# Kernel tuning notes

Measured on AMD Instinct MI355X. Metric: run time of the kernel, lower is better.

Reference implementation:

```python
import jax, jax.numpy as jnp
import numpy as np

N = 100000   # num_labels
E = 3200000  # num edges
F_IN, H1, H2 = 384, 128, 64


def setup_inputs() -> dict:
    key = jax.random.key(0)
    k0, k1, k2, k3 = jax.random.split(key, 4)
    x = jax.random.normal(k0, (N, F_IN), dtype=jnp.float32) * 0.05
    W1 = jax.random.normal(k1, (F_IN, H1), dtype=jnp.float32) * (1.0 / np.sqrt(F_IN))
    b1 = jnp.zeros((H1,), dtype=jnp.float32)
    W2 = jax.random.normal(k2, (H1, H2), dtype=jnp.float32) * (1.0 / np.sqrt(H1))
    b2 = jnp.zeros((H2,), dtype=jnp.float32)
    edge_index = jax.random.randint(k3, (2, E), 0, N, dtype=jnp.int32)
    return {"x": x, "W1": W1, "b1": b1, "W2": W2, "b2": b2, "edge_index": edge_index}


def _gcn_norm(edge_index, num_nodes):
    # PyG gcn_norm: add self loops, deg from dst with unit weights, sym norm.
    loops = jnp.arange(num_nodes, dtype=edge_index.dtype)
    src = jnp.concatenate([edge_index[0], loops])
    dst = jnp.concatenate([edge_index[1], loops])
    deg = jax.ops.segment_sum(jnp.ones_like(dst, dtype=jnp.float32), dst,
                              num_segments=num_nodes)
    dis = jnp.where(deg > 0, jax.lax.rsqrt(deg), 0.0)
    norm = dis[src] * dis[dst]  # [E + N]
    return src, dst, norm


def _gcn_conv(x, W, b, src, dst, norm, num_nodes):
    h = x @ W                                   # [N, out]
    msg = h[src] * norm[:, None]                # gather + scale
    out = jax.ops.segment_sum(msg, dst, num_segments=num_nodes)
    return out + b


def reference(x, W1, b1, W2, b2, edge_index):
    src, dst, norm = _gcn_norm(edge_index, N)
    h = jax.nn.relu(_gcn_conv(x, W1, b1, src, dst, norm, N))
    out = _gcn_conv(h, W2, b2, src, dst, norm, N)
    return out
```

## Files before the change

### kernel.cpp

```cpp
#include <hip/hip_runtime.h>
#include <hip/hip_fp16.h>
#include <math.h>

#define N_NODES 100000
#define N_EDGES 3200000
#define F_IN    384
#define H1      128
#define H2      64

#define NBKT    782
#define HIST_W  800
#define NB_BIN  256
#define EPB     (N_EDGES / NB_BIN)


__global__ __launch_bounds__(256) void k_hist(const int* __restrict__ dst,
                                              int* __restrict__ hist) {
    __shared__ int h[HIST_W];
    int b = blockIdx.x, t = threadIdx.x;
    for (int i = t; i < HIST_W; i += 256) h[i] = 0;
    __syncthreads();
    int e0 = b * EPB, e1 = e0 + EPB;
    for (int e = e0 + t; e < e1; e += 256)
        atomicAdd(&h[dst[e] >> 7], 1);
    __syncthreads();
    for (int i = t; i < HIST_W; i += 256) hist[b * HIST_W + i] = h[i];
}


__global__ __launch_bounds__(1024) void k_scan_off(int* __restrict__ hist,
                                                   int* __restrict__ bucketBase) {
    __shared__ int s[1024];
    int t = threadIdx.x;
    int run = 0;
    if (t < HIST_W) {
        #pragma unroll 8
        for (int b = 0; b < NB_BIN; b++) {
            int v = hist[b * HIST_W + t];
            hist[b * HIST_W + t] = run;
            run += v;
        }
    }
    int tot = (t < NBKT) ? run : 0;
    s[t] = tot; __syncthreads();
    for (int off = 1; off < 1024; off <<= 1) {
        int x = (t >= off) ? s[t - off] : 0;
        __syncthreads();
        s[t] += x;
        __syncthreads();
    }
    if (t <= NBKT) bucketBase[t] = s[t] - tot;
}


__global__ __launch_bounds__(256) void k_bin(const int* __restrict__ src,
                                             const int* __restrict__ dst,
                                             const int* __restrict__ hist,
                                             const int* __restrict__ bucketBase,
                                             int* __restrict__ binned) {
    __shared__ int lcur[HIST_W];
    int b = blockIdx.x, t = threadIdx.x;
    for (int i = t; i < HIST_W; i += 256)
        lcur[i] = ((i < NBKT) ? bucketBase[i] : 0) + hist[b * HIST_W + i];
    __syncthreads();
    int e0 = b * EPB, e1 = e0 + EPB;
    for (int e = e0 + t; e < e1; e += 256) {
        int d = dst[e];
        int p = atomicAdd(&lcur[d >> 7], 1);
        binned[p] = ((d & 127) << 17) | src[e];
    }
}


__global__ __launch_bounds__(256) void k_build(const int* __restrict__ binned,
                                               const int* __restrict__ bucketBase,
                                               int* __restrict__ csr,
                                               int* __restrict__ offsets,
                                               int* __restrict__ ecnt,
                                               float* __restrict__ dis) {
    __shared__ int ldeg[128], spre[128], lcur[128];
    int bkt = blockIdx.x, t = threadIdx.x;
    int e0 = bucketBase[bkt], e1 = bucketBase[bkt + 1];
    if (t < 128) ldeg[t] = 0;
    __syncthreads();
    for (int e = e0 + t; e < e1; e += 256)
        atomicAdd(&ldeg[binned[e] >> 17], 1);
    __syncthreads();
    int v = (t < 128) ? ldeg[t] : 0;
    if (t < 128) spre[t] = v;
    __syncthreads();
    for (int off = 1; off < 128; off <<= 1) {
        int x = (t < 128 && t >= off) ? spre[t - off] : 0;
        __syncthreads();
        if (t < 128) spre[t] += x;
        __syncthreads();
    }
    if (t < 128) {
        int node = bkt * 128 + t;
        if (node < N_NODES) {
            int base = e0 + spre[t] - v;
            offsets[node] = base;
            ecnt[node]    = v;
            dis[node]     = rsqrtf((float)(v + 1));
            lcur[t]       = base;
        }
    }
    __syncthreads();
    for (int e = e0 + t; e < e1; e += 256) {
        int p = binned[e];
        int pos = atomicAdd(&lcur[p >> 17], 1);
        csr[pos] = p & 0x1FFFF;
    }
}


__global__ __launch_bounds__(256) void k_gemm1(const float* __restrict__ x,
                                               const float* __restrict__ W1,
                                               const float* __restrict__ dis,
                                               __half* __restrict__ hs1) {
    __shared__ float xl[16][72];
    __shared__ float wl[16][128];
    int t = threadIdx.x;
    int m0 = blockIdx.x * 64;
    int tr = t >> 5, tc = t & 31;
    float acc[8][4] = {};
    for (int k0 = 0; k0 < F_IN; k0 += 16) {
        {
            int r = t >> 2, kq = (t & 3) * 4;
            int rr = m0 + r; if (rr >= N_NODES) rr = N_NODES - 1;
            float4 a = *(const float4*)&x[(size_t)rr * F_IN + k0 + kq];
            xl[kq][r] = a.x; xl[kq + 1][r] = a.y; xl[kq + 2][r] = a.z; xl[kq + 3][r] = a.w;
        }
        #pragma unroll
        for (int jj = 0; jj < 2; jj++) {
            int idx = t + jj * 256;
            int k = idx >> 5, c4 = idx & 31;
            *(float4*)&wl[k][c4 * 4] = *(const float4*)&W1[(size_t)(k0 + k) * H1 + c4 * 4];
        }
        __syncthreads();
        #pragma unroll
        for (int kk = 0; kk < 16; kk++) {
            float4 a0 = *(const float4*)&xl[kk][tr * 8];
            float4 a1 = *(const float4*)&xl[kk][tr * 8 + 4];
            float4 b  = *(const float4*)&wl[kk][tc * 4];
            float av[8] = {a0.x, a0.y, a0.z, a0.w, a1.x, a1.y, a1.z, a1.w};
            float bv[4] = {b.x, b.y, b.z, b.w};
            #pragma unroll
            for (int i = 0; i < 8; i++)
                #pragma unroll
                for (int u = 0; u < 4; u++)
                    acc[i][u] += av[i] * bv[u];
        }
        __syncthreads();
    }
    #pragma unroll
    for (int i = 0; i < 8; i++) {
        int row = m0 + tr * 8 + i;
        if (row < N_NODES) {
            float dr = dis[row];
            __half2* o2 = (__half2*)&hs1[(size_t)row * H1 + tc * 4];
            o2[0] = __floats2half2_rn(acc[i][0] * dr, acc[i][1] * dr);
            o2[1] = __floats2half2_rn(acc[i][2] * dr, acc[i][3] * dr);
        }
    }
}


__global__ __launch_bounds__(256) void k_agg1(const __half* __restrict__ hs1,
                                              const float* __restrict__ dis,
                                              const int* __restrict__ csr,
                                              const int* __restrict__ offsets,
                                              const int* __restrict__ ecnt,
                                              const float* __restrict__ b1,
                                              float* __restrict__ hr) {
    int w = (blockIdx.x * 256 + threadIdx.x) >> 6;
    if (w >= N_NODES) return;
    int lane = threadIdx.x & 63;
    int j = lane * 2;
    const __half2* __restrict__ h = (const __half2*)hs1;
    float di = dis[w];
    int start = offsets[w];
    int cnt = ecnt[w];
    float2 selfv = __half22float2(h[(size_t)w * 64 + lane]);
    float sx = selfv.x;
    float sy = selfv.y;
    for (int k = 0; k < cnt; k += 8) {
        int s[8]; __half2 v[8];
        #pragma unroll
        for (int u = 0; u < 8; u++) {
            int kk = k + u;
            s[u] = csr[start + (kk < cnt ? kk : cnt - 1)];
        }
        #pragma unroll
        for (int u = 0; u < 8; u++)
            v[u] = h[(size_t)s[u] * 64 + lane];
        #pragma unroll
        for (int u = 0; u < 8; u++) {
            float2 f = __half22float2(v[u]);
            bool ok = (k + u < cnt);
            sx += ok ? f.x : 0.f;
            sy += ok ? f.y : 0.f;
        }
    }
    float2 bb = *(const float2*)&b1[j];
    float2 o = make_float2(fmaxf(bb.x + di * sx, 0.f),
                           fmaxf(bb.y + di * sy, 0.f));
    *(float2*)&hr[(size_t)w * H1 + j] = o;
}


__global__ __launch_bounds__(256) void k_gemm2(const float* __restrict__ hr,
                                               const float* __restrict__ W2,
                                               const float* __restrict__ dis,
                                               __half* __restrict__ hs2) {
    __shared__ float hl[32][128];
    __shared__ float wl[128][64];
    int t = threadIdx.x;
    int m0 = blockIdx.x * 32;
    #pragma unroll
    for (int j = 0; j < 8; j++) {
        int i4 = t + j * 256;
        int r = i4 >> 4, c4 = i4 & 15;
        *(float4*)&wl[r][c4 * 4] = *(const float4*)&W2[(size_t)r * H2 + c4 * 4];
    }
    #pragma unroll
    for (int j = 0; j < 4; j++) {
        int i4 = t + j * 256;
        int r = i4 >> 5, c4 = i4 & 31;
        *(float4*)&hl[r][c4 * 4] = *(const float4*)&hr[(size_t)(m0 + r) * H1 + c4 * 4];
    }
    __syncthreads();
    int c = t & 63, rg = t >> 6;
    float acc[8] = {};
    for (int k = 0; k < H1; k++) {
        float wv = wl[k][c];
        #pragma unroll
        for (int i = 0; i < 8; i++) acc[i] += hl[rg * 8 + i][k] * wv;
    }
    #pragma unroll
    for (int i = 0; i < 8; i++) {
        int row = m0 + rg * 8 + i;
        hs2[(size_t)row * H2 + c] = __float2half_rn(dis[row] * acc[i]);
    }
}


__global__ __launch_bounds__(256) void k_agg2(const __half* __restrict__ hs2,
                                              const float* __restrict__ dis,
                                              const int* __restrict__ csr,
                                              const int* __restrict__ offsets,
                                              const int* __restrict__ ecnt,
                                              const float* __restrict__ b2,
                                              float* __restrict__ out) {
    int w = (blockIdx.x * 256 + threadIdx.x) >> 6;
    if (w >= N_NODES) return;
    int lane = threadIdx.x & 63;
    float di = dis[w];
    int start = offsets[w];
    int cnt = ecnt[w];
    float acc = __half2float(hs2[(size_t)w * H2 + lane]);
    for (int k = 0; k < cnt; k += 8) {
        int s[8]; __half v[8];
        #pragma unroll
        for (int u = 0; u < 8; u++) {
            int kk = k + u;
            s[u] = csr[start + (kk < cnt ? kk : cnt - 1)];
        }
        #pragma unroll
        for (int u = 0; u < 8; u++)
            v[u] = hs2[(size_t)s[u] * H2 + lane];
        #pragma unroll
        for (int u = 0; u < 8; u++) {
            float f = __half2float(v[u]);
            acc += (k + u < cnt) ? f : 0.f;
        }
    }
    out[(size_t)w * H2 + lane] = b2[lane] + di * acc;
}


extern "C" void kernel_launch(void* const* d_in, const int* in_sizes, int n_in,
                              void* d_out, int out_size, void* d_ws, size_t ws_size,
                              hipStream_t stream) {
    const float* x  = (const float*)d_in[0];
    const float* W1 = (const float*)d_in[1];
    const float* b1 = (const float*)d_in[2];
    const float* W2 = (const float*)d_in[3];
    const float* b2 = (const float*)d_in[4];
    const int*   ei = (const int*)d_in[5];
    const int* src = ei;
    const int* dst = ei + N_EDGES;
    float* out = (float*)d_out;

    char* ws = (char*)d_ws;
    float* dis        = (float*)ws; ws += (size_t)N_NODES * 4;
    int*   offsets    = (int*)ws;   ws += (size_t)N_NODES * 4;
    int*   ecnt       = (int*)ws;   ws += (size_t)N_NODES * 4;
    int*   bucketBase = (int*)ws;   ws += 1024 * 4;
    int*   hist       = (int*)ws;   ws += (size_t)NB_BIN * HIST_W * 4;
    int*   csr        = (int*)ws;   ws += (size_t)N_EDGES * 4;
    __half* hs1       = (__half*)ws; ws += (size_t)N_NODES * H1 * 2;
    float* hr         = (float*)ws; ws += (size_t)N_NODES * H1 * 4;
    int*   binned     = (int*)hr;
    __half* hs2       = hs1;

    k_hist    <<<NB_BIN, 256, 0, stream>>>(dst, hist);
    k_scan_off<<<1, 1024, 0, stream>>>(hist, bucketBase);
    k_bin     <<<NB_BIN, 256, 0, stream>>>(src, dst, hist, bucketBase, binned);
    k_build   <<<NBKT, 256, 0, stream>>>(binned, bucketBase, csr, offsets, ecnt, dis);

    k_gemm1<<<(N_NODES + 63) / 64, 256, 0, stream>>>(x, W1, dis, hs1);
    k_agg1<<<(N_NODES + 3) / 4, 256, 0, stream>>>(hs1, dis, csr, offsets, ecnt, b1, hr);
    k_gemm2<<<N_NODES / 32, 256, 0, stream>>>(hr, W2, dis, hs2);
    k_agg2<<<(N_NODES + 3) / 4, 256, 0, stream>>>(hs2, dis, csr, offsets, ecnt, b2, out);
}
```

Measured before the change: 689.4 us.

## Use fp16 MFMA for first GEMM with pre-transposed half-precision W1

```diff
diff --git a/kernel.cpp b/kernel.cpp
--- a/kernel.cpp
+++ b/kernel.cpp
@@ -12,6 +12,9 @@
 #define HIST_W  800
 #define NB_BIN  256
 #define EPB     (N_EDGES / NB_BIN)
+
+typedef _Float16 f16x8 __attribute__((ext_vector_type(8)));
+typedef float    f32x4 __attribute__((ext_vector_type(4)));
 
 
 __global__ __launch_bounds__(256) void k_hist(const int* __restrict__ dst,
@@ -114,53 +117,78 @@
 }
 
 
+__global__ __launch_bounds__(256) void k_w1t(const float* __restrict__ W1,
+                                             __half* __restrict__ w1t) {
+    int id = blockIdx.x * 256 + threadIdx.x;
+    int c = id / F_IN, k = id % F_IN;
+    w1t[id] = __float2half_rn(W1[(size_t)k * H1 + c]);
+}
+
+
 __global__ __launch_bounds__(256) void k_gemm1(const float* __restrict__ x,
-                                               const float* __restrict__ W1,
+                                               const __half* __restrict__ w1t,
                                                const float* __restrict__ dis,
                                                __half* __restrict__ hs1) {
-    __shared__ float xl[16][72];
-    __shared__ float wl[16][128];
+    __shared__ f16x8 xl[512];
+    __shared__ f16x8 wt[1024];
     int t = threadIdx.x;
     int m0 = blockIdx.x * 64;
-    int tr = t >> 5, tc = t & 31;
-    float acc[8][4] = {};
-    for (int k0 = 0; k0 < F_IN; k0 += 16) {
-        {
-            int r = t >> 2, kq = (t & 3) * 4;
-            int rr = m0 + r; if (rr >= N_NODES) rr = N_NODES - 1;
-            float4 a = *(const float4*)&x[(size_t)rr * F_IN + k0 + kq];
-            xl[kq][r] = a.x; xl[kq + 1][r] = a.y; xl[kq + 2][r] = a.z; xl[kq + 3][r] = a.w;
-        }
-        #pragma unroll
-        for (int jj = 0; jj < 2; jj++) {
-            int idx = t + jj * 256;
-            int k = idx >> 5, c4 = idx & 31;
-            *(float4*)&wl[k][c4 * 4] = *(const float4*)&W1[(size_t)(k0 + k) * H1 + c4 * 4];
-        }
-        __syncthreads();
-        #pragma unroll
-        for (int kk = 0; kk < 16; kk++) {
-            float4 a0 = *(const float4*)&xl[kk][tr * 8];
-            float4 a1 = *(const float4*)&xl[kk][tr * 8 + 4];
-            float4 b  = *(const float4*)&wl[kk][tc * 4];
-            float av[8] = {a0.x, a0.y, a0.z, a0.w, a1.x, a1.y, a1.z, a1.w};
-            float bv[4] = {b.x, b.y, b.z, b.w};
+    int wv = t >> 6, l = t & 63;
+    int lrow = l & 15, kg = l >> 4;
+    f32x4 acc[8];
+    #pragma unroll
+    for (int nb = 0; nb < 8; nb++) acc[nb] = (f32x4){0.f, 0.f, 0.f, 0.f};
+
+    char* xb = (char*)xl;
+    char* wb = (char*)wt;
+
+    for (int k0 = 0; k0 < F_IN; k0 += 64) {
+        #pragma unroll
+        for (int j = 0; j < 2; j++) {
+            int s = t + j * 256;
+            int r = s >> 3, kc = (s & 7) * 8;
+            int rg = m0 + r; if (rg >= N_NODES) rg = N_NODES - 1;
+            const float* px = &x[(size_t)rg * F_IN + k0 + kc];
+            float4 p0 = *(const float4*)px;
+            float4 p1 = *(const float4*)(px + 4);
+            f16x8 h;
+            h[0] = (_Float16)p0.x; h[1] = (_Float16)p0.y;
+            h[2] = (_Float16)p0.z; h[3] = (_Float16)p0.w;
+            h[4] = (_Float16)p1.x; h[5] = (_Float16)p1.y;
+            h[6] = (_Float16)p1.z; h[7] = (_Float16)p1.w;
+            *(f16x8*)(xb + ((r * 128 + kc * 2) ^ ((r & 7) << 4))) = h;
+        }
+        #pragma unroll
+        for (int j = 0; j < 4; j++) {
+            int s = t + j * 256;
+            int c = s >> 3, kc = (s & 7) * 8;
+            f16x8 h = *(const f16x8*)&w1t[(size_t)c * F_IN + k0 + kc];
+            *(f16x8*)(wb + ((c * 128 + kc * 2) ^ ((c & 7) << 4))) = h;
+        }
+        __syncthreads();
+        #pragma unroll
+        for (int ks = 0; ks < 2; ks++) {
+            int r = wv * 16 + lrow;
+            int kb = (ks * 32 + kg * 8) * 2;
+            f16x8 a = *(const f16x8*)(xb + ((r * 128 + kb) ^ ((r & 7) << 4)));
             #pragma unroll
-            for (int i = 0; i < 8; i++)
-                #pragma unroll
-                for (int u = 0; u < 4; u++)
-                    acc[i][u] += av[i] * bv[u];
-        }
-        __syncthreads();
-    }
-    #pragma unroll
-    for (int i = 0; i < 8; i++) {
-        int row = m0 + tr * 8 + i;
+            for (int nb = 0; nb < 8; nb++) {
+                int c = nb * 16 + lrow;
+                f16x8 b = *(const f16x8*)(wb + ((c * 128 + kb) ^ ((c & 7) << 4)));
+                acc[nb] = __builtin_amdgcn_mfma_f32_16x16x32_f16(a, b, acc[nb], 0, 0, 0);
+            }
+        }
+        __syncthreads();
+    }
+    int rbase = m0 + wv * 16 + kg * 4;
+    #pragma unroll
+    for (int reg = 0; reg < 4; reg++) {
+        int row = rbase + reg;
         if (row < N_NODES) {
             float dr = dis[row];
-            __half2* o2 = (__half2*)&hs1[(size_t)row * H1 + tc * 4];
-            o2[0] = __floats2half2_rn(acc[i][0] * dr, acc[i][1] * dr);
-            o2[1] = __floats2half2_rn(acc[i][2] * dr, acc[i][3] * dr);
+            #pragma unroll
+            for (int nb = 0; nb < 8; nb++)
+                hs1[(size_t)row * H1 + nb * 16 + lrow] = __float2half_rn(acc[nb][reg] * dr);
         }
     }
 }
@@ -299,17 +327,19 @@
     int*   bucketBase = (int*)ws;   ws += 1024 * 4;
     int*   hist       = (int*)ws;   ws += (size_t)NB_BIN * HIST_W * 4;
     int*   csr        = (int*)ws;   ws += (size_t)N_EDGES * 4;
+    __half* w1t       = (__half*)ws; ws += (size_t)H1 * F_IN * 2;
     __half* hs1       = (__half*)ws; ws += (size_t)N_NODES * H1 * 2;
     float* hr         = (float*)ws; ws += (size_t)N_NODES * H1 * 4;
     int*   binned     = (int*)hr;
     __half* hs2       = hs1;
 
+    k_w1t     <<<(H1 * F_IN) / 256, 256, 0, stream>>>(W1, w1t);
     k_hist    <<<NB_BIN, 256, 0, stream>>>(dst, hist);
     k_scan_off<<<1, 1024, 0, stream>>>(hist, bucketBase);
     k_bin     <<<NB_BIN, 256, 0, stream>>>(src, dst, hist, bucketBase, binned);
     k_build   <<<NBKT, 256, 0, stream>>>(binned, bucketBase, csr, offsets, ecnt, dis);
 
-    k_gemm1<<<(N_NODES + 63) / 64, 256, 0, stream>>>(x, W1, dis, hs1);
+    k_gemm1<<<(N_NODES + 63) / 64, 256, 0, stream>>>(x, w1t, dis, hs1);
     k_agg1<<<(N_NODES + 3) / 4, 256, 0, stream>>>(hs1, dis, csr, offsets, ecnt, b1, hr);
     k_gemm2<<<N_NODES / 32, 256, 0, stream>>>(hr, W2, dis, hs2);
     k_agg2<<<(N_NODES + 3) / 4, 256, 0, stream>>>(hs2, dis, csr, offsets, ecnt, b2, out);
```

Measured after the change: 634.6 us. 1.09x faster.
